# Optimization experiments

Hardware: AMD Instinct MI355X
Metric: run time of the kernel (lower is better)

The kernel has to match this reference:

```python
import jax, jax.numpy as jnp
import numpy as np

N_NODES = 100000
N_EDGES = 1600000
IN_DIM = 500
HID = 32
N_REL = 7
OUT_DIM = 4
N_GRAPHS = 16


def setup_inputs() -> dict:
    key = jax.random.key(0)
    ks = jax.random.split(key, 9)
    node_x = jax.random.normal(ks[0], (N_NODES, IN_DIM), dtype=jnp.float32)
    edge_index = jax.random.randint(ks[1], (2, N_EDGES), 0, N_NODES, dtype=jnp.int64)
    edge_attr = jax.random.randint(ks[2], (N_EDGES,), 0, N_REL, dtype=jnp.int64)
    batch = jnp.sort(jax.random.randint(ks[3], (N_NODES,), 0, N_GRAPHS, dtype=jnp.int64))
    # learned params (RGCNConv: per-relation weight, root weight, bias; then fc)
    s_in = 1.0 / np.sqrt(IN_DIM)
    W_rel = jax.random.uniform(ks[4], (N_REL, IN_DIM, HID), jnp.float32, -s_in, s_in)
    W_root = jax.random.uniform(ks[5], (IN_DIM, HID), jnp.float32, -s_in, s_in)
    bias = jnp.zeros((HID,), jnp.float32)
    s_h = 1.0 / np.sqrt(HID)
    fc_w = jax.random.uniform(ks[6], (HID, OUT_DIM), jnp.float32, -s_h, s_h)
    fc_b = jax.random.uniform(ks[7], (OUT_DIM,), jnp.float32, -s_h, s_h)
    return {"node_x": node_x, "edge_index": edge_index, "edge_attr": edge_attr,
            "batch": batch, "W_rel": W_rel, "W_root": W_root, "bias": bias,
            "fc_w": fc_w, "fc_b": fc_b}


def _rgcn(node_x, edge_index, edge_attr, W_rel, W_root, bias):
    # PyG RGCNConv with default aggr='mean': per-relation mean over incoming
    # edges, summed across relations, plus root transform and bias.
    src, dst = edge_index[0], edge_index[1]
    out = node_x @ W_root + bias  # [N, HID]
    for r in range(N_REL):
        h = node_x @ W_rel[r]                       # [N, HID] transform first (cheap: HID << IN_DIM)
        m = (edge_attr == r).astype(node_x.dtype)   # [E] relation mask
        msg = h[src] * m[:, None]                   # [E, HID]
        s = jax.ops.segment_sum(msg, dst, num_segments=N_NODES)
        cnt = jax.ops.segment_sum(m, dst, num_segments=N_NODES)
        out = out + s / jnp.maximum(cnt, 1.0)[:, None]
    return out


def reference(node_x, edge_index, edge_attr, batch, W_rel, W_root, bias, fc_w, fc_b):
    x = _rgcn(node_x, edge_index, edge_attr, W_rel, W_root, bias)
    x = jax.nn.relu(x)
    # global_add_pool over per-node graph ids
    pooled = jax.ops.segment_sum(x, batch, num_segments=N_GRAPHS)  # [B, HID]
    return pooled @ fc_w + fc_b  # [B, OUT_DIM]
```

## Files before the change

### kernel.cpp

```cpp
#include <hip/hip_runtime.h>

#define N_NODES 100000
#define N_EDGES 1600000
#define IN_DIM 500
#define HID 32
#define N_REL 7
#define OUT_DIM 4
#define N_GRAPHS 16
#define NC 256
#define MC 224
#define KPAD 512

#define BK_SHIFT 6
#define BK_NODES 64
#define N_BUCKETS ((N_NODES + BK_NODES - 1) / BK_NODES)
#define NSUB 8
#define SUB_CAP 256
#define BK_CAP (NSUB * SUB_CAP)
#define NPOOL 8

typedef __attribute__((ext_vector_type(8))) short bf16x8;
typedef __attribute__((ext_vector_type(4))) float f32x4;

__device__ inline unsigned short f2bf(float f) {
    unsigned u = __float_as_uint(f);
    unsigned r = (u + 0x7FFFu + ((u >> 16) & 1u)) >> 16;
    return (unsigned short)r;
}
__device__ inline float bf2f(unsigned short b) {
    return __uint_as_float((unsigned)b << 16);
}

__global__ void build_wbf(const float* __restrict__ W_root,
                          const float* __restrict__ W_rel,
                          unsigned short* __restrict__ Wbf) {
    int idx = blockIdx.x * blockDim.x + threadIdx.x;
    if (idx >= KPAD * NC) return;
    int kk = idx >> 8;
    int n = idx & 255;
    float v = 0.f;
    if (kk < IN_DIM) {
        if (n < HID) v = W_root[kk * HID + n];
        else {
            int r = (n >> 5) - 1;
            v = W_rel[((size_t)r * IN_DIM + kk) * HID + (n & 31)];
        }
    }
    int ks = kk >> 5, q = (kk >> 3) & 3, j = kk & 7;
    Wbf[(size_t)((((ks << 2) + q) << 8) + n) * 8 + j] = f2bf(v);
}

__global__ __launch_bounds__(256, 4) void gemm_mfma(const float* __restrict__ A,
                                                    const uint4* __restrict__ Wbf,
                                                    float* __restrict__ Hr,
                                                    unsigned short* __restrict__ Hm) {
    __shared__ uint4 Alds[32 * 64];

    const int tid = threadIdx.x;
    const int wave = tid >> 6, lane = tid & 63;
    const int l16 = lane & 15, q = lane >> 4;
    const int row0 = blockIdx.x * 64;
    const int wn = wave * 64;

    int rows_valid = N_NODES - row0; if (rows_valid > 64) rows_valid = 64;
    const float4* Ablk4 = (const float4*)(A + (size_t)row0 * IN_DIM);

    f32x4 acc[4][4];
    #pragma unroll
    for (int mt = 0; mt < 4; mt++)
        #pragma unroll
        for (int nt = 0; nt < 4; nt++)
            #pragma unroll
            for (int r = 0; r < 4; r++) acc[mt][nt][r] = 0.f;

    for (int half = 0; half < 2; half++) {
        if (half) __syncthreads();
        #pragma unroll 4
        for (int it = 0; it < 16; it++) {
            int idx = it * 256 + tid;
            int row = idx >> 6, slot = idx & 63;
            int k = half * 256 + slot * 4;
            float4 v = make_float4(0.f, 0.f, 0.f, 0.f);
            if (row < rows_valid && k < IN_DIM)
                v = Ablk4[row * 125 + (k >> 2)];
            int ksq = slot >> 1;
            int e = (ksq << 6) | ((row ^ ksq) & 63);
            ushort4 b;
            b.x = f2bf(v.x); b.y = f2bf(v.y); b.z = f2bf(v.z); b.w = f2bf(v.w);
            *(ushort4*)((unsigned short*)&Alds[e] + (slot & 1) * 4) = b;
        }
        __syncthreads();
        #pragma unroll 2
        for (int ksl = 0; ksl < 8; ksl++) {
            int ksq_l = ksl * 4 + q;
            int ksq_g = half * 32 + ksq_l;
            bf16x8 bfr[4], afr[4];
            #pragma unroll
            for (int nt = 0; nt < 4; nt++) {
                uint4 t = Wbf[(size_t)(ksq_g << 8) + wn + nt * 16 + l16];
                bfr[nt] = *(bf16x8*)&t;
            }
            #pragma unroll
            for (int mt = 0; mt < 4; mt++)
                afr[mt] = *(const bf16x8*)&Alds[(ksq_l << 6) | (((mt * 16 + l16) ^ ksq_l) & 63)];
            #pragma unroll
            for (int mt = 0; mt < 4; mt++)
                #pragma unroll
                for (int nt = 0; nt < 4; nt++)
                    acc[mt][nt] = __builtin_amdgcn_mfma_f32_16x16x32_bf16(
                        afr[mt], bfr[nt], acc[mt][nt], 0, 0, 0);
        }
    }

    #pragma unroll
    for (int mt = 0; mt < 4; mt++) {
        int rbase = row0 + mt * 16 + q * 4;
        #pragma unroll
        for (int r = 0; r < 4; r++) {
            int row = rbase + r;
            if (row < N_NODES) {
                #pragma unroll
                for (int nt = 0; nt < 4; nt++) {
                    int col = wn + nt * 16 + l16;
                    float v = acc[mt][nt][r];
                    if (wave == 0 && nt < 2)
                        Hr[(size_t)row * HID + col] = v;
                    else
                        Hm[(size_t)row * MC + (col - HID)] = f2bf(v);
                }
            }
        }
    }
}

__global__ void init_bcur(int* __restrict__ bcur) {
    int i = blockIdx.x * blockDim.x + threadIdx.x;
    if (i < N_BUCKETS * NSUB) bcur[i] = i * SUB_CAP;
}

__global__ __launch_bounds__(256) void bin_edges(const int* __restrict__ src,
                                                 const int* __restrict__ dst,
                                                 const int* __restrict__ attr,
                                                 int* __restrict__ bcur,
                                                 int* __restrict__ rec) {
    int e = blockIdx.x * blockDim.x + threadIdx.x;
    if (e >= N_EDGES) return;
    int d = dst[e];
    int cur = (d >> BK_SHIFT) * NSUB + (blockIdx.x & (NSUB - 1));
    int p = atomicAdd(&bcur[cur], 1);
    if (p < (cur + 1) * SUB_CAP)
        rec[p] = ((d & (BK_NODES - 1)) << 20) | (src[e] << 3) | attr[e];
}

__global__ __launch_bounds__(256) void bucket_sort(int* __restrict__ rec,
                                                   const int* __restrict__ bcur,
                                                   int* __restrict__ deg,
                                                   int* __restrict__ offs,
                                                   float* __restrict__ invcnt) {
    __shared__ int h2[BK_NODES * N_REL];
    __shared__ int lcur[BK_NODES];
    __shared__ int sorted[BK_CAP];
    __shared__ int scnt[NSUB];
    __shared__ int s_total;

    const int b = blockIdx.x, t = threadIdx.x;
    const int n0 = b << BK_SHIFT;
    const size_t rbase = (size_t)b * BK_CAP;

    for (int i = t; i < BK_NODES * N_REL; i += 256) h2[i] = 0;
    if (t < NSUB) {
        int c = bcur[b * NSUB + t] - (b * NSUB + t) * SUB_CAP;
        scnt[t] = c < SUB_CAP ? c : SUB_CAP;
    }
    __syncthreads();

    for (int s = 0; s < NSUB; s++) {
        int cs = scnt[s];
        const int* rp = rec + rbase + s * SUB_CAP;
        for (int i = t; i < cs; i += 256) {
            int q = rp[i];
            atomicAdd(&h2[(q >> 20) * N_REL + (q & 7)], 1);
        }
    }
    __syncthreads();

    if (t < BK_NODES) {
        int tot = 0;
        #pragma unroll
        for (int r = 0; r < N_REL; r++) tot += h2[t * N_REL + r];
        int incl = tot;
        #pragma unroll
        for (int off = 1; off < BK_NODES; off <<= 1) {
            int y = __shfl_up(incl, off, 64);
            if (t >= off) incl += y;
        }
        int excl = incl - tot;
        lcur[t] = excl;
        if (t == BK_NODES - 1) s_total = incl;
        int n = n0 + t;
        if (n < N_NODES) {
            deg[n] = tot;
            offs[n] = (int)rbase + excl;
        }
    }
    int lim = (N_NODES - n0) * N_REL;
    if (lim > BK_NODES * N_REL) lim = BK_NODES * N_REL;
    for (int i = t; i < lim; i += 256) {
        int cc = h2[i];
        invcnt[(size_t)n0 * N_REL + i] = 1.0f / (float)(cc > 1 ? cc : 1);
    }
    __syncthreads();

    for (int s = 0; s < NSUB; s++) {
        int cs = scnt[s];
        const int* rp = rec + rbase + s * SUB_CAP;
        for (int i = t; i < cs; i += 256) {
            int q = rp[i];
            int p = atomicAdd(&lcur[q >> 20], 1);
            if (p < BK_CAP)
                sorted[p] = q & 0xFFFFF;
        }
    }
    __syncthreads();

    int total = s_total;
    if (total > BK_CAP) total = BK_CAP;
    for (int i = t; i < total; i += 256) rec[rbase + i] = sorted[i];
}

__global__ __launch_bounds__(256) void gather_agg(const int* __restrict__ rec,
                                                  const int* __restrict__ offs,
                                                  const int* __restrict__ deg,
                                                  const float* __restrict__ invcnt,
                                                  const float* __restrict__ bias,
                                                  const unsigned short* __restrict__ Hm,
                                                  const float* __restrict__ Hr,
                                                  const int* __restrict__ batch,
                                                  float* __restrict__ pooled) {
    __shared__ float lpool[N_GRAPHS][HID];
    const int t = threadIdx.x;
    for (int i = t; i < N_GRAPHS * HID; i += 256) ((float*)lpool)[i] = 0.f;
    __syncthreads();

    const int d = blockIdx.x * 8 + (t >> 5);
    const int c = t & 31;

    int dg = deg[d];
    int start = offs[d];
    int end = start + dg;

    float acc = 0.f;
    int i = start;
    for (; i + 7 < end; i += 8) {
        int q0 = rec[i], q1 = rec[i + 1], q2 = rec[i + 2], q3 = rec[i + 3];
        int q4 = rec[i + 4], q5 = rec[i + 5], q6 = rec[i + 6], q7 = rec[i + 7];
        float h0 = bf2f(Hm[(size_t)(q0 >> 3) * MC + (q0 & 7) * HID + c]);
        float h1 = bf2f(Hm[(size_t)(q1 >> 3) * MC + (q1 & 7) * HID + c]);
        float h2 = bf2f(Hm[(size_t)(q2 >> 3) * MC + (q2 & 7) * HID + c]);
        float h3 = bf2f(Hm[(size_t)(q3 >> 3) * MC + (q3 & 7) * HID + c]);
        float h4 = bf2f(Hm[(size_t)(q4 >> 3) * MC + (q4 & 7) * HID + c]);
        float h5 = bf2f(Hm[(size_t)(q5 >> 3) * MC + (q5 & 7) * HID + c]);
        float h6 = bf2f(Hm[(size_t)(q6 >> 3) * MC + (q6 & 7) * HID + c]);
        float h7 = bf2f(Hm[(size_t)(q7 >> 3) * MC + (q7 & 7) * HID + c]);
        acc = fmaf(h0, invcnt[d * N_REL + (q0 & 7)], acc);
        acc = fmaf(h1, invcnt[d * N_REL + (q1 & 7)], acc);
        acc = fmaf(h2, invcnt[d * N_REL + (q2 & 7)], acc);
        acc = fmaf(h3, invcnt[d * N_REL + (q3 & 7)], acc);
        acc = fmaf(h4, invcnt[d * N_REL + (q4 & 7)], acc);
        acc = fmaf(h5, invcnt[d * N_REL + (q5 & 7)], acc);
        acc = fmaf(h6, invcnt[d * N_REL + (q6 & 7)], acc);
        acc = fmaf(h7, invcnt[d * N_REL + (q7 & 7)], acc);
    }
    for (; i < end; i++) {
        int qq = rec[i];
        acc = fmaf(bf2f(Hm[(size_t)(qq >> 3) * MC + (qq & 7) * HID + c]),
                   invcnt[d * N_REL + (qq & 7)], acc);
    }

    float v = Hr[(size_t)d * HID + c] + bias[c] + acc;
    v = fmaxf(v, 0.f);
    atomicAdd(&lpool[batch[d]][c], v);
    __syncthreads();

    float* pp = pooled + (size_t)(blockIdx.x & (NPOOL - 1)) * N_GRAPHS * HID;
    for (int i2 = t; i2 < N_GRAPHS * HID; i2 += 256) {
        float v2 = ((float*)lpool)[i2];
        if (v2 != 0.f) atomicAdd(&pp[i2], v2);
    }
}

__global__ void fc_kernel(const float* __restrict__ pooled, const float* __restrict__ fc_w,
                          const float* __restrict__ fc_b, float* __restrict__ out) {
    int t = threadIdx.x;
    if (t >= N_GRAPHS * OUT_DIM) return;
    int g = t >> 2, o = t & 3;
    float acc = fc_b[o];
    #pragma unroll
    for (int c = 0; c < HID; c++) {
        float p = 0.f;
        #pragma unroll
        for (int k = 0; k < NPOOL; k++)
            p += pooled[(size_t)(k * N_GRAPHS + g) * HID + c];
        acc += p * fc_w[c * OUT_DIM + o];
    }
    out[t] = acc;
}

extern "C" void kernel_launch(void* const* d_in, const int* in_sizes, int n_in,
                              void* d_out, int out_size, void* d_ws, size_t ws_size,
                              hipStream_t stream) {
    const float* node_x  = (const float*)d_in[0];
    const int*   edge_ix = (const int*)d_in[1];
    const int*   e_attr  = (const int*)d_in[2];
    const int*   batch   = (const int*)d_in[3];
    const float* W_rel   = (const float*)d_in[4];
    const float* W_root  = (const float*)d_in[5];
    const float* bias    = (const float*)d_in[6];
    const float* fc_w    = (const float*)d_in[7];
    const float* fc_b    = (const float*)d_in[8];
    float* out = (float*)d_out;

    char* ws = (char*)d_ws;
    size_t off = 0;
    auto alloc = [&](size_t bytes) {
        char* p = ws + off;
        off += (bytes + 255) & ~(size_t)255;
        return p;
    };
    unsigned short* Wbf = (unsigned short*)alloc((size_t)KPAD * NC * 2);
    float* Hr      = (float*)alloc((size_t)N_NODES * HID * 4);
    unsigned short* Hm = (unsigned short*)alloc((size_t)N_NODES * MC * 2);
    int*   rec     = (int*)  alloc((size_t)N_BUCKETS * BK_CAP * 4);
    int*   bcur    = (int*)  alloc((size_t)N_BUCKETS * NSUB * 4);
    int*   deg     = (int*)  alloc((size_t)N_NODES * 4);
    int*   offsb   = (int*)  alloc((size_t)N_NODES * 4);
    float* invcnt  = (float*)alloc((size_t)N_NODES * N_REL * 4);
    float* pooled  = (float*)alloc((size_t)NPOOL * N_GRAPHS * HID * 4);
    (void)ws_size; (void)in_sizes; (void)n_in; (void)out_size;

    const int* src = edge_ix;
    const int* dst = edge_ix + N_EDGES;

    hipMemsetAsync(pooled, 0, (size_t)NPOOL * N_GRAPHS * HID * 4, stream);

    build_wbf<<<(KPAD * NC + 255) / 256, 256, 0, stream>>>(W_root, W_rel, Wbf);

    init_bcur<<<(N_BUCKETS * NSUB + 255) / 256, 256, 0, stream>>>(bcur);
    bin_edges<<<(N_EDGES + 255) / 256, 256, 0, stream>>>(src, dst, e_attr, bcur, rec);
    bucket_sort<<<N_BUCKETS, 256, 0, stream>>>(rec, bcur, deg, offsb, invcnt);

    gemm_mfma<<<(N_NODES + 63) / 64, 256, 0, stream>>>(node_x, (const uint4*)Wbf, Hr, Hm);

    gather_agg<<<(N_NODES + 7) / 8, 256, 0, stream>>>(rec, offsb, deg, invcnt,
                                                      bias, Hm, Hr, batch, pooled);

    fc_kernel<<<1, 64, 0, stream>>>(pooled, fc_w, fc_b, out);
}
```

Baseline: 491.8 us.

## Double-buffer GEMM A tiles with register prefetch and predicate gather tail

The GEMM kernel now stages A in four 128-wide K chunks. Global loads for the next chunk go into registers while the current chunk's MFMAs run, and LDS is double-buffered. Weight fragments are also prefetched one k-step ahead. Together these hide global-load latency behind the matrix math, at the cost of more registers, so launch bounds drop from 4 to 3 blocks per CU. Separately, the aggregation kernel replaces its unrolled-by-8 loop plus scalar tail with a single predicated 8-wide loop. The masked lanes read rec past the segment end, which may read beyond the end of the array for the last node.

After: 500.6 us. About the same (+1.8%).

```diff
diff --git a/kernel.cpp b/kernel.cpp
--- a/kernel.cpp
+++ b/kernel.cpp
@@ -50,11 +50,11 @@
     Wbf[(size_t)((((ks << 2) + q) << 8) + n) * 8 + j] = f2bf(v);
 }
 
-__global__ __launch_bounds__(256, 4) void gemm_mfma(const float* __restrict__ A,
+__global__ __launch_bounds__(256, 3) void gemm_mfma(const float* __restrict__ A,
                                                     const uint4* __restrict__ Wbf,
                                                     float* __restrict__ Hr,
                                                     unsigned short* __restrict__ Hm) {
-    __shared__ uint4 Alds[32 * 64];
+    __shared__ uint4 Alds[2][16 * 64];
 
     const int tid = threadIdx.x;
     const int wave = tid >> 6, lane = tid & 63;
@@ -65,6 +65,34 @@
     int rows_valid = N_NODES - row0; if (rows_valid > 64) rows_valid = 64;
     const float4* Ablk4 = (const float4*)(A + (size_t)row0 * IN_DIM);
 
+    float4 sreg[8];
+
+    auto issue = [&](int c) {
+        #pragma unroll
+        for (int j = 0; j < 8; j++) {
+            int idx = j * 256 + tid;
+            int row = idx >> 5, slot = idx & 31;
+            int k = c * 128 + slot * 4;
+            float4 v = make_float4(0.f, 0.f, 0.f, 0.f);
+            if (row < rows_valid && k < IN_DIM)
+                v = Ablk4[row * 125 + (k >> 2)];
+            sreg[j] = v;
+        }
+    };
+    auto commit = [&](int c) {
+        #pragma unroll
+        for (int j = 0; j < 8; j++) {
+            int idx = j * 256 + tid;
+            int row = idx >> 5, slot = idx & 31;
+            int ksq = slot >> 1;
+            int e = (ksq << 6) | ((row ^ ksq) & 63);
+            ushort4 b;
+            b.x = f2bf(sreg[j].x); b.y = f2bf(sreg[j].y);
+            b.z = f2bf(sreg[j].z); b.w = f2bf(sreg[j].w);
+            *(ushort4*)((unsigned short*)&Alds[c & 1][e] + (slot & 1) * 4) = b;
+        }
+    };
+
     f32x4 acc[4][4];
     #pragma unroll
     for (int mt = 0; mt < 4; mt++)
@@ -73,42 +101,51 @@
             #pragma unroll
             for (int r = 0; r < 4; r++) acc[mt][nt][r] = 0.f;
 
-    for (int half = 0; half < 2; half++) {
-        if (half) __syncthreads();
-        #pragma unroll 4
-        for (int it = 0; it < 16; it++) {
-            int idx = it * 256 + tid;
-            int row = idx >> 6, slot = idx & 63;
-            int k = half * 256 + slot * 4;
-            float4 v = make_float4(0.f, 0.f, 0.f, 0.f);
-            if (row < rows_valid && k < IN_DIM)
-                v = Ablk4[row * 125 + (k >> 2)];
-            int ksq = slot >> 1;
-            int e = (ksq << 6) | ((row ^ ksq) & 63);
-            ushort4 b;
-            b.x = f2bf(v.x); b.y = f2bf(v.y); b.z = f2bf(v.z); b.w = f2bf(v.w);
-            *(ushort4*)((unsigned short*)&Alds[e] + (slot & 1) * 4) = b;
-        }
-        __syncthreads();
-        #pragma unroll 2
-        for (int ksl = 0; ksl < 8; ksl++) {
+    issue(0);
+    commit(0);
+    issue(1);
+    __syncthreads();
+
+    for (int c = 0; c < 4; c++) {
+        bf16x8 bnxt[4];
+        {
+            int kg = c * 16 + q;
+            #pragma unroll
+            for (int nt = 0; nt < 4; nt++) {
+                uint4 t = Wbf[(size_t)(kg << 8) + wn + nt * 16 + l16];
+                bnxt[nt] = *(bf16x8*)&t;
+            }
+        }
+        #pragma unroll
+        for (int ksl = 0; ksl < 4; ksl++) {
+            bf16x8 bcur[4];
+            #pragma unroll
+            for (int nt = 0; nt < 4; nt++) bcur[nt] = bnxt[nt];
+            if (ksl < 3) {
+                int kg = c * 16 + (ksl + 1) * 4 + q;
+                #pragma unroll
+                for (int nt = 0; nt < 4; nt++) {
+                    uint4 t = Wbf[(size_t)(kg << 8) + wn + nt * 16 + l16];
+                    bnxt[nt] = *(bf16x8*)&t;
+                }
+            }
             int ksq_l = ksl * 4 + q;
-            int ksq_g = half * 32 + ksq_l;
-            bf16x8 bfr[4], afr[4];
-            #pragma unroll
-            for (int nt = 0; nt < 4; nt++) {
-                uint4 t = Wbf[(size_t)(ksq_g << 8) + wn + nt * 16 + l16];
-                bfr[nt] = *(bf16x8*)&t;
-            }
+            bf16x8 afr[4];
             #pragma unroll
             for (int mt = 0; mt < 4; mt++)
-                afr[mt] = *(const bf16x8*)&Alds[(ksq_l << 6) | (((mt * 16 + l16) ^ ksq_l) & 63)];
+                afr[mt] = *(const bf16x8*)&Alds[c & 1]
+                    [(ksq_l << 6) | (((mt * 16 + l16) ^ ksq_l) & 63)];
             #pragma unroll
             for (int mt = 0; mt < 4; mt++)
                 #pragma unroll
                 for (int nt = 0; nt < 4; nt++)
                     acc[mt][nt] = __builtin_amdgcn_mfma_f32_16x16x32_bf16(
-                        afr[mt], bfr[nt], acc[mt][nt], 0, 0, 0);
+                        afr[mt], bcur[nt], acc[mt][nt], 0, 0, 0);
+        }
+        if (c < 3) {
+            commit(c + 1);
+            if (c < 2) issue(c + 2);
+            __syncthreads();
         }
     }
 
@@ -250,31 +287,22 @@
     int end = start + dg;
 
     float acc = 0.f;
-    int i = start;
-    for (; i + 7 < end; i += 8) {
-        int q0 = rec[i], q1 = rec[i + 1], q2 = rec[i + 2], q3 = rec[i + 3];
-        int q4 = rec[i + 4], q5 = rec[i + 5], q6 = rec[i + 6], q7 = rec[i + 7];
-        float h0 = bf2f(Hm[(size_t)(q0 >> 3) * MC + (q0 & 7) * HID + c]);
-        float h1 = bf2f(Hm[(size_t)(q1 >> 3) * MC + (q1 & 7) * HID + c]);
-        float h2 = bf2f(Hm[(size_t)(q2 >> 3) * MC + (q2 & 7) * HID + c]);
-        float h3 = bf2f(Hm[(size_t)(q3 >> 3) * MC + (q3 & 7) * HID + c]);
-        float h4 = bf2f(Hm[(size_t)(q4 >> 3) * MC + (q4 & 7) * HID + c]);
-        float h5 = bf2f(Hm[(size_t)(q5 >> 3) * MC + (q5 & 7) * HID + c]);
-        float h6 = bf2f(Hm[(size_t)(q6 >> 3) * MC + (q6 & 7) * HID + c]);
-        float h7 = bf2f(Hm[(size_t)(q7 >> 3) * MC + (q7 & 7) * HID + c]);
-        acc = fmaf(h0, invcnt[d * N_REL + (q0 & 7)], acc);
-        acc = fmaf(h1, invcnt[d * N_REL + (q1 & 7)], acc);
-        acc = fmaf(h2, invcnt[d * N_REL + (q2 & 7)], acc);
-        acc = fmaf(h3, invcnt[d * N_REL + (q3 & 7)], acc);
-        acc = fmaf(h4, invcnt[d * N_REL + (q4 & 7)], acc);
-        acc = fmaf(h5, invcnt[d * N_REL + (q5 & 7)], acc);
-        acc = fmaf(h6, invcnt[d * N_REL + (q6 & 7)], acc);
-        acc = fmaf(h7, invcnt[d * N_REL + (q7 & 7)], acc);
-    }
-    for (; i < end; i++) {
-        int qq = rec[i];
-        acc = fmaf(bf2f(Hm[(size_t)(qq >> 3) * MC + (qq & 7) * HID + c]),
-                   invcnt[d * N_REL + (qq & 7)], acc);
+    for (int i = start; i < end; i += 8) {
+        int q[8];
+        float h[8], w[8];
+        #pragma unroll
+        for (int j = 0; j < 8; j++) {
+            bool ok = (i + j) < end;
+            int qq = rec[i + j];
+            q[j] = ok ? qq : 0;
+            w[j] = ok ? 1.f : 0.f;
+        }
+        #pragma unroll
+        for (int j = 0; j < 8; j++)
+            h[j] = bf2f(Hm[(size_t)((q[j] >> 3) & 0x1FFFF) * MC + (q[j] & 7) * HID + c]);
+        #pragma unroll
+        for (int j = 0; j < 8; j++)
+            acc = fmaf(h[j], w[j] * invcnt[d * N_REL + (q[j] & 7)], acc);
     }
 
     float v = Hr[(size_t)d * HID + c] + bias[c] + acc;
```

## Merge edge binning into GEMM kernel and fold init kernels into weight build

Applied to the files above, without the earlier changes.

Edge binning now runs inside the same launch as the bf16 MFMA GEMM: block groups are interleaved so one in five groups does GEMM tiles and the rest bin edges. The goal is to overlap the memory-bound, atomic-heavy binning with the bandwidth-heavy GEMM. The bcur init and pooled memset move into build_wbf, removing two launches. The gather loop is also rewritten as a predicated 8-wide unroll with no scalar tail. The mixed grid wastes some blocks and may change GEMM occupancy or cache behaviour, and the masked loop reads rec entries past the end of a node's range (weighted to zero).

Result: faster. 425.8 us (-13.4%).

```diff
diff --git a/kernel.cpp b/kernel.cpp
--- a/kernel.cpp
+++ b/kernel.cpp
@@ -19,6 +19,11 @@
 #define BK_CAP (NSUB * SUB_CAP)
 #define NPOOL 8
 
+#define GEMM_BLOCKS ((N_NODES + 63) / 64)
+#define BIN_BLOCKS  ((N_EDGES + 255) / 256)
+#define N_GROUPS 978
+#define GRID_MERGED (N_GROUPS * 8)
+
 typedef __attribute__((ext_vector_type(8))) short bf16x8;
 typedef __attribute__((ext_vector_type(4))) float f32x4;
 
@@ -33,8 +38,12 @@
 
 __global__ void build_wbf(const float* __restrict__ W_root,
                           const float* __restrict__ W_rel,
-                          unsigned short* __restrict__ Wbf) {
+                          unsigned short* __restrict__ Wbf,
+                          int* __restrict__ bcur,
+                          float* __restrict__ pooled) {
     int idx = blockIdx.x * blockDim.x + threadIdx.x;
+    if (idx < N_BUCKETS * NSUB) bcur[idx] = idx * SUB_CAP;
+    if (idx < NPOOL * N_GRAPHS * HID) pooled[idx] = 0.f;
     if (idx >= KPAD * NC) return;
     int kk = idx >> 8;
     int n = idx & 255;
@@ -50,16 +59,39 @@
     Wbf[(size_t)((((ks << 2) + q) << 8) + n) * 8 + j] = f2bf(v);
 }
 
-__global__ __launch_bounds__(256, 4) void gemm_mfma(const float* __restrict__ A,
-                                                    const uint4* __restrict__ Wbf,
-                                                    float* __restrict__ Hr,
-                                                    unsigned short* __restrict__ Hm) {
+__global__ __launch_bounds__(256, 4) void gemm_bin(const float* __restrict__ A,
+                                                   const uint4* __restrict__ Wbf,
+                                                   float* __restrict__ Hr,
+                                                   unsigned short* __restrict__ Hm,
+                                                   const int* __restrict__ src,
+                                                   const int* __restrict__ dst,
+                                                   const int* __restrict__ attr,
+                                                   int* __restrict__ bcur,
+                                                   int* __restrict__ rec) {
+    const int grp = blockIdx.x >> 3, j8 = blockIdx.x & 7;
+
+    if (grp % 5 != 0) {
+        int bb = (grp - grp / 5 - 1) * 8 + j8;
+        if (bb >= BIN_BLOCKS) return;
+        int e = bb * 256 + threadIdx.x;
+        if (e >= N_EDGES) return;
+        int d = dst[e];
+        int cur = (d >> BK_SHIFT) * NSUB + j8;
+        int p = atomicAdd(&bcur[cur], 1);
+        if (p < (cur + 1) * SUB_CAP)
+            rec[p] = ((d & (BK_NODES - 1)) << 20) | (src[e] << 3) | attr[e];
+        return;
+    }
+
+    int bid = (grp / 5) * 8 + j8;
+    if (bid >= GEMM_BLOCKS) return;
+
     __shared__ uint4 Alds[32 * 64];
 
     const int tid = threadIdx.x;
     const int wave = tid >> 6, lane = tid & 63;
     const int l16 = lane & 15, q = lane >> 4;
-    const int row0 = blockIdx.x * 64;
+    const int row0 = bid * 64;
     const int wn = wave * 64;
 
     int rows_valid = N_NODES - row0; if (rows_valid > 64) rows_valid = 64;
@@ -133,25 +165,6 @@
     }
 }
 
-__global__ void init_bcur(int* __restrict__ bcur) {
-    int i = blockIdx.x * blockDim.x + threadIdx.x;
-    if (i < N_BUCKETS * NSUB) bcur[i] = i * SUB_CAP;
-}
-
-__global__ __launch_bounds__(256) void bin_edges(const int* __restrict__ src,
-                                                 const int* __restrict__ dst,
-                                                 const int* __restrict__ attr,
-                                                 int* __restrict__ bcur,
-                                                 int* __restrict__ rec) {
-    int e = blockIdx.x * blockDim.x + threadIdx.x;
-    if (e >= N_EDGES) return;
-    int d = dst[e];
-    int cur = (d >> BK_SHIFT) * NSUB + (blockIdx.x & (NSUB - 1));
-    int p = atomicAdd(&bcur[cur], 1);
-    if (p < (cur + 1) * SUB_CAP)
-        rec[p] = ((d & (BK_NODES - 1)) << 20) | (src[e] << 3) | attr[e];
-}
-
 __global__ __launch_bounds__(256) void bucket_sort(int* __restrict__ rec,
                                                    const int* __restrict__ bcur,
                                                    int* __restrict__ deg,
@@ -250,31 +263,22 @@
     int end = start + dg;
 
     float acc = 0.f;
-    int i = start;
-    for (; i + 7 < end; i += 8) {
-        int q0 = rec[i], q1 = rec[i + 1], q2 = rec[i + 2], q3 = rec[i + 3];
-        int q4 = rec[i + 4], q5 = rec[i + 5], q6 = rec[i + 6], q7 = rec[i + 7];
-        float h0 = bf2f(Hm[(size_t)(q0 >> 3) * MC + (q0 & 7) * HID + c]);
-        float h1 = bf2f(Hm[(size_t)(q1 >> 3) * MC + (q1 & 7) * HID + c]);
-        float h2 = bf2f(Hm[(size_t)(q2 >> 3) * MC + (q2 & 7) * HID + c]);
-        float h3 = bf2f(Hm[(size_t)(q3 >> 3) * MC + (q3 & 7) * HID + c]);
-        float h4 = bf2f(Hm[(size_t)(q4 >> 3) * MC + (q4 & 7) * HID + c]);
-        float h5 = bf2f(Hm[(size_t)(q5 >> 3) * MC + (q5 & 7) * HID + c]);
-        float h6 = bf2f(Hm[(size_t)(q6 >> 3) * MC + (q6 & 7) * HID + c]);
-        float h7 = bf2f(Hm[(size_t)(q7 >> 3) * MC + (q7 & 7) * HID + c]);
-        acc = fmaf(h0, invcnt[d * N_REL + (q0 & 7)], acc);
-        acc = fmaf(h1, invcnt[d * N_REL + (q1 & 7)], acc);
-        acc = fmaf(h2, invcnt[d * N_REL + (q2 & 7)], acc);
-        acc = fmaf(h3, invcnt[d * N_REL + (q3 & 7)], acc);
-        acc = fmaf(h4, invcnt[d * N_REL + (q4 & 7)], acc);
-        acc = fmaf(h5, invcnt[d * N_REL + (q5 & 7)], acc);
-        acc = fmaf(h6, invcnt[d * N_REL + (q6 & 7)], acc);
-        acc = fmaf(h7, invcnt[d * N_REL + (q7 & 7)], acc);
-    }
-    for (; i < end; i++) {
-        int qq = rec[i];
-        acc = fmaf(bf2f(Hm[(size_t)(qq >> 3) * MC + (qq & 7) * HID + c]),
-                   invcnt[d * N_REL + (qq & 7)], acc);
+    for (int i = start; i < end; i += 8) {
+        int q[8];
+        float h[8], w[8];
+        #pragma unroll
+        for (int j = 0; j < 8; j++) {
+            bool ok = (i + j) < end;
+            int qq = rec[i + j];
+            q[j] = ok ? qq : 0;
+            w[j] = ok ? 1.f : 0.f;
+        }
+        #pragma unroll
+        for (int j = 0; j < 8; j++)
+            h[j] = bf2f(Hm[(size_t)((q[j] >> 3) & 0x1FFFF) * MC + (q[j] & 7) * HID + c]);
+        #pragma unroll
+        for (int j = 0; j < 8; j++)
+            acc = fmaf(h[j], w[j] * invcnt[d * N_REL + (q[j] & 7)], acc);
     }
 
     float v = Hr[(size_t)d * HID + c] + bias[c] + acc;
@@ -341,15 +345,13 @@
     const int* src = edge_ix;
     const int* dst = edge_ix + N_EDGES;
 
-    hipMemsetAsync(pooled, 0, (size_t)NPOOL * N_GRAPHS * HID * 4, stream);
-
-    build_wbf<<<(KPAD * NC + 255) / 256, 256, 0, stream>>>(W_root, W_rel, Wbf);
-
-    init_bcur<<<(N_BUCKETS * NSUB + 255) / 256, 256, 0, stream>>>(bcur);
-    bin_edges<<<(N_EDGES + 255) / 256, 256, 0, stream>>>(src, dst, e_attr, bcur, rec);
+    build_wbf<<<(KPAD * NC + 255) / 256, 256, 0, stream>>>(W_root, W_rel, Wbf,
+                                                           bcur, pooled);
+
+    gemm_bin<<<GRID_MERGED, 256, 0, stream>>>(node_x, (const uint4*)Wbf, Hr, Hm,
+                                              src, dst, e_attr, bcur, rec);
+
     bucket_sort<<<N_BUCKETS, 256, 0, stream>>>(rec, bcur, deg, offsb, invcnt);
-
-    gemm_mfma<<<(N_NODES + 63) / 64, 256, 0, stream>>>(node_x, (const uint4*)Wbf, Hr, Hm);
 
     gather_agg<<<(N_NODES + 7) / 8, 256, 0, stream>>>(rec, offsb, deg, invcnt,
                                                       bias, Hm, Hr, batch, pooled);
```
